# Kernel optimization log

Measured on AMD Instinct MI355X. Metric: run time of the kernel, lower is better.

The kernel has to match this reference:

```python
import jax, jax.numpy as jnp
import numpy as np

VOCAB = 1024
D = 1024  # predictor_dim
B = 32
U = 512
NULL_INDEX = 0


def setup_inputs() -> dict:
    key = jax.random.key(0)
    ks = jax.random.split(key, 9)
    s = 1.0 / np.sqrt(D)
    return {
        "y": jax.random.randint(ks[0], (B, U), 0, VOCAB, dtype=jnp.int32),
        "embed_table": jax.random.normal(ks[1], (VOCAB, D), jnp.float32) * s,
        "Wx": jax.random.normal(ks[2], (D, 3 * D), jnp.float32) * s,  # input kernel [z|r|h]
        "Wh": jax.random.normal(ks[3], (D, 3 * D), jnp.float32) * s,  # recurrent kernel [z|r|h]
        "bx": jnp.zeros((3 * D,), jnp.float32),  # input bias (reset_after=True)
        "bh": jnp.zeros((3 * D,), jnp.float32),  # recurrent bias (reset_after=True)
        "Wd": jax.random.normal(ks[4], (D, D), jnp.float32) * s,
        "bd": jnp.zeros((D,), jnp.float32),
        "h0": jax.random.normal(ks[5], (D,), jnp.float32),  # self.initial_state
    }


def _gru_scan(tokens, embed_table, Wx, Wh, bx, bh, h0_b):
    # tokens: [B, T] int; returns hidden states [B, T, D]
    x = embed_table[tokens]                       # [B, T, D]
    # Precompute all input projections outside the recurrence (one big GEMM)
    xp = jnp.einsum("btd,de->bte", x, Wx) + bx    # [B, T, 3D]
    xp = jnp.moveaxis(xp, 1, 0)                   # [T, B, 3D]

    def step(h, xp_t):
        hp = h @ Wh + bh                          # [B, 3D], reset_after=True
        xz, xr, xh = jnp.split(xp_t, 3, axis=-1)
        hz, hr, hh = jnp.split(hp, 3, axis=-1)
        z = jax.nn.sigmoid(xz + hz)
        r = jax.nn.sigmoid(xr + hr)
        hcand = jnp.tanh(xh + r * hh)
        h_new = z * h + (1.0 - z) * hcand
        return h_new, h_new

    _, hs = jax.lax.scan(step, h0_b, xp)          # hs: [T, B, D]
    return jnp.moveaxis(hs, 0, 1)                 # [B, T, D]


def reference(y, embed_table, Wx, Wh, bx, bh, Wd, bd, h0):
    Bn = y.shape[0]
    start = jnp.full((Bn, 1), NULL_INDEX, dtype=y.dtype)
    tokens = jnp.concatenate([start, y], axis=1)  # [B, U+1]
    h0_b = jnp.broadcast_to(h0, (Bn, D))
    hs = _gru_scan(tokens, embed_table, Wx, Wh, bx, bh, h0_b)  # [B, U+1, D]
    outs = jnp.einsum("btd,de->bte", hs, Wd) + bd
    return outs
```

## Files before the change

### kernel.cpp

```cpp
#include <hip/hip_runtime.h>
#include <hip/hip_bf16.h>
#include <cstdint>

typedef __bf16 bf16;
typedef __bf16 bf16x8 __attribute__((ext_vector_type(8)));
typedef float  f32x4  __attribute__((ext_vector_type(4)));
typedef uint32_t u32x4 __attribute__((ext_vector_type(4)));

#define D_DIM   1024
#define ND      3072
#define B_SZ    32
#define U_SZ    512
#define T_SZ    513
#define M_REAL  (B_SZ * T_SZ)
#define WXS_LD  1032
#define A_LD    1032
#define XP_LD   20

#define AGENT __HIP_MEMORY_SCOPE_AGENT

__device__ __forceinline__ f32x4 mfma16(bf16x8 a, bf16x8 b, f32x4 c) {
    return __builtin_amdgcn_mfma_f32_16x16x32_bf16(a, b, c, 0, 0, 0);
}

struct bfpair { bf16x8 hi, lo; };

__device__ __forceinline__ bfpair split8(const float* p) {
    f32x4 a = *(const f32x4*)p;
    f32x4 b = *(const f32x4*)(p + 4);
    bfpair r;
#pragma unroll
    for (int j = 0; j < 4; ++j) {
        r.hi[j] = (bf16)a[j];
        r.lo[j] = (bf16)(a[j] - (float)r.hi[j]);
        r.hi[4 + j] = (bf16)b[j];
        r.lo[4 + j] = (bf16)(b[j] - (float)r.hi[4 + j]);
    }
    return r;
}

__device__ __forceinline__ bf16x8 cvt8(const float* p) {
    f32x4 a = *(const f32x4*)p;
    f32x4 b = *(const f32x4*)(p + 4);
    bf16x8 r;
#pragma unroll
    for (int j = 0; j < 4; ++j) { r[j] = (bf16)a[j]; r[4 + j] = (bf16)b[j]; }
    return r;
}

__device__ __forceinline__ bfpair unpack8(const uint32_t* p) {
    u32x4 a = *(const u32x4*)p;
    u32x4 b = *(const u32x4*)(p + 4);
    union { uint32_t u[4]; bf16x8 v; } H, L;
    H.u[0] = __builtin_amdgcn_perm(a.y, a.x, 0x05040100u);
    H.u[1] = __builtin_amdgcn_perm(a.w, a.z, 0x05040100u);
    H.u[2] = __builtin_amdgcn_perm(b.y, b.x, 0x05040100u);
    H.u[3] = __builtin_amdgcn_perm(b.w, b.z, 0x05040100u);
    L.u[0] = __builtin_amdgcn_perm(a.y, a.x, 0x07060302u);
    L.u[1] = __builtin_amdgcn_perm(a.w, a.z, 0x07060302u);
    L.u[2] = __builtin_amdgcn_perm(b.y, b.x, 0x07060302u);
    L.u[3] = __builtin_amdgcn_perm(b.w, b.z, 0x07060302u);
    bfpair r; r.hi = H.v; r.lo = L.v;
    return r;
}

__global__ void transpose_split(const float* __restrict__ in,
                                bf16* __restrict__ out_hi, bf16* __restrict__ out_lo,
                                int R, int C) {
    __shared__ float tile[32][33];
    const int c0 = blockIdx.x * 32, r0 = blockIdx.y * 32;
    const int tx = threadIdx.x, ty = threadIdx.y;
    for (int i = 0; i < 32; i += 8)
        tile[ty + i][tx] = in[(size_t)(r0 + ty + i) * C + c0 + tx];
    __syncthreads();
    for (int i = 0; i < 32; i += 8) {
        const float v  = tile[tx][ty + i];
        const bf16  hi = (bf16)v;
        out_hi[(size_t)(c0 + ty + i) * R + r0 + tx] = hi;
        out_lo[(size_t)(c0 + ty + i) * R + r0 + tx] = (bf16)(v - (float)hi);
    }
}

__global__ __launch_bounds__(256, 1)
void gru_scan(const float* __restrict__ Wx,    const float* __restrict__ Wh,
              const float* __restrict__ bx,    const float* __restrict__ bh,
              const float* __restrict__ h0,    const float* __restrict__ embed,
              const int* __restrict__ y,       uint32_t* __restrict__ ghs,
              int* __restrict__ flags)
{
    __shared__ __align__(16) bf16 WxS[48 * WXS_LD];
    __shared__ __align__(16) float xpx[2][96 * XP_LD];
    __shared__ __align__(16) float bxs[3][16], bhs[3][16];

    const int tid  = threadIdx.x;
    const int wave = tid >> 6, lane = tid & 63;
    const int quad = lane >> 4, l15 = lane & 15;
    const int n0 = blockIdx.x * 16;
    int* slots = flags;

    for (int idx = tid; idx < 3 * 1024 * 16; idx += 256) {
        const int cl = idx & 15;
        const int k  = (idx >> 4) & 1023;
        const int g  = idx >> 14;
        WxS[(g * 16 + cl) * WXS_LD + k] = (bf16)Wx[(size_t)k * ND + g * D_DIM + n0 + cl];
    }
    if (tid < 48) {
        bxs[tid >> 4][tid & 15] = bx[(tid >> 4) * D_DIM + n0 + (tid & 15)];
        bhs[tid >> 4][tid & 15] = bh[(tid >> 4) * D_DIM + n0 + (tid & 15)];
    }

    bf16x8 bregZ[32], bregR[32], bregH[32];
    if (wave < 2) {
#pragma unroll
        for (int ks = 0; ks < 32; ++ks) {
            bf16x8 vz, vr, vh;
#pragma unroll
            for (int j = 0; j < 8; ++j) {
                const size_t krow = (size_t)(ks * 32 + quad * 8 + j) * ND + n0 + l15;
                vz[j] = (bf16)Wh[krow];
                vr[j] = (bf16)Wh[krow + D_DIM];
                vh[j] = (bf16)Wh[krow + 2 * D_DIM];
            }
            bregZ[ks] = vz; bregR[ks] = vr; bregH[ks] = vh;
        }
    }

    const int batch = (wave & 1) * 16 + l15;
    f32x4 holdv = *(const f32x4*)(h0 + n0 + quad * 4);
    unsigned long long junk = 0;

    __syncthreads();

    if (wave >= 2) {
        const float* xrow = embed + quad * 8;
        f32x4 ax0 = {}, ax1 = {}, ax2 = {};
#pragma unroll
        for (int ks = 0; ks < 32; ++ks) {
            bf16x8 xa = cvt8(xrow + ks * 32);
            bf16x8 w0 = *(const bf16x8*)(WxS + (l15)      * WXS_LD + ks * 32 + quad * 8);
            bf16x8 w1 = *(const bf16x8*)(WxS + (16 + l15) * WXS_LD + ks * 32 + quad * 8);
            bf16x8 w2 = *(const bf16x8*)(WxS + (32 + l15) * WXS_LD + ks * 32 + quad * 8);
            ax0 = mfma16(w0, xa, ax0);
            ax1 = mfma16(w1, xa, ax1);
            ax2 = mfma16(w2, xa, ax2);
        }
        *(f32x4*)(xpx[0] + (batch)      * XP_LD + quad * 4) = ax0;
        *(f32x4*)(xpx[0] + (32 + batch) * XP_LD + quad * 4) = ax1;
        *(f32x4*)(xpx[0] + (64 + batch) * XP_LD + quad * 4) = ax2;
    }
    __syncthreads();

    for (int t = 0; t < T_SZ; ++t) {
        if (wave < 2) {
            f32x4 azh = {}, azl = {}, arh = {}, arl = {}, ahh = {}, ahl = {};
            if (t == 0) {
                const float* hrow = h0 + quad * 8;
#pragma unroll
                for (int ks = 0; ks < 32; ++ks) {
                    bfpair h8 = split8(hrow + ks * 32);
                    azh = mfma16(bregZ[ks], h8.hi, azh);
                    azl = mfma16(bregZ[ks], h8.lo, azl);
                    arh = mfma16(bregR[ks], h8.hi, arh);
                    arl = mfma16(bregR[ks], h8.lo, arl);
                    ahh = mfma16(bregH[ks], h8.hi, ahh);
                    ahl = mfma16(bregH[ks], h8.lo, ahl);
                }
            } else {
                const uint32_t* hrow = ghs
                    + ((size_t)batch * T_SZ + (t - 1)) * D_DIM + quad * 8;
#pragma unroll
                for (int ks = 0; ks < 32; ++ks) {
                    bfpair h8 = unpack8(hrow + ks * 32);
                    azh = mfma16(bregZ[ks], h8.hi, azh);
                    azl = mfma16(bregZ[ks], h8.lo, azl);
                    arh = mfma16(bregR[ks], h8.hi, arh);
                    arl = mfma16(bregR[ks], h8.lo, arl);
                    ahh = mfma16(bregH[ks], h8.hi, ahh);
                    ahl = mfma16(bregH[ks], h8.lo, ahl);
                }
            }

            const int p = t & 1;
            const f32x4 xz = *(const f32x4*)(xpx[p] + (batch)      * XP_LD + quad * 4);
            const f32x4 xr = *(const f32x4*)(xpx[p] + (32 + batch) * XP_LD + quad * 4);
            const f32x4 xh = *(const f32x4*)(xpx[p] + (64 + batch) * XP_LD + quad * 4);
            const f32x4 bxz = *(const f32x4*)(&bxs[0][quad * 4]);
            const f32x4 bxr = *(const f32x4*)(&bxs[1][quad * 4]);
            const f32x4 bxh = *(const f32x4*)(&bxs[2][quad * 4]);
            const f32x4 bhz = *(const f32x4*)(&bhs[0][quad * 4]);
            const f32x4 bhr = *(const f32x4*)(&bhs[1][quad * 4]);
            const f32x4 bhh = *(const f32x4*)(&bhs[2][quad * 4]);
            uint32_t pk[4];
#pragma unroll
            for (int i = 0; i < 4; ++i) {
                const float hz  = azh[i] + azl[i] + bhz[i];
                const float hr  = arh[i] + arl[i] + bhr[i];
                const float hhv = ahh[i] + ahl[i] + bhh[i];
                const float z  = 1.f / (1.f + __expf(-(xz[i] + bxz[i] + hz)));
                const float r  = 1.f / (1.f + __expf(-(xr[i] + bxr[i] + hr)));
                const float pa = xh[i] + bxh[i] + r * hhv;
                const float hc = 1.f - 2.f / (__expf(2.f * pa) + 1.f);
                const float hn = z * holdv[i] + (1.f - z) * hc;
                holdv[i] = hn;
                const bf16 hi = (bf16)hn;
                const bf16 lo = (bf16)(hn - (float)hi);
                pk[i] = (uint32_t)__builtin_bit_cast(uint16_t, hi)
                      | ((uint32_t)__builtin_bit_cast(uint16_t, lo) << 16);
            }
            const unsigned long long e0 = (unsigned long long)pk[0]
                                        | ((unsigned long long)pk[1] << 32);
            const unsigned long long e1 = (unsigned long long)pk[2]
                                        | ((unsigned long long)pk[3] << 32);
            unsigned long long* dst = (unsigned long long*)
                (ghs + ((size_t)batch * T_SZ + t) * D_DIM + n0 + quad * 4);
            junk ^= __hip_atomic_exchange(dst,     e0, __ATOMIC_RELAXED, AGENT);
            junk ^= __hip_atomic_exchange(dst + 1, e1, __ATOMIC_RELAXED, AGENT);
        } else if (t < U_SZ) {
            const int tok = y[batch * U_SZ + t] & 1023;
            const float* xrow = embed + (size_t)tok * D_DIM + quad * 8;
            const int p = (t + 1) & 1;
            f32x4 ax0 = {}, ax1 = {}, ax2 = {};
#pragma unroll
            for (int ks = 0; ks < 32; ++ks) {
                bf16x8 xa = cvt8(xrow + ks * 32);
                bf16x8 w0 = *(const bf16x8*)(WxS + (l15)      * WXS_LD + ks * 32 + quad * 8);
                bf16x8 w1 = *(const bf16x8*)(WxS + (16 + l15) * WXS_LD + ks * 32 + quad * 8);
                bf16x8 w2 = *(const bf16x8*)(WxS + (32 + l15) * WXS_LD + ks * 32 + quad * 8);
                ax0 = mfma16(w0, xa, ax0);
                ax1 = mfma16(w1, xa, ax1);
                ax2 = mfma16(w2, xa, ax2);
            }
            *(f32x4*)(xpx[p] + (batch)      * XP_LD + quad * 4) = ax0;
            *(f32x4*)(xpx[p] + (32 + batch) * XP_LD + quad * 4) = ax1;
            *(f32x4*)(xpx[p] + (64 + batch) * XP_LD + quad * 4) = ax2;
        }

        __syncthreads();

        if (t + 1 < T_SZ) {
            const int tv = t + 1;
            if (tid == 0)
                __hip_atomic_store(slots + (blockIdx.x << 4), tv,
                                   __ATOMIC_RELAXED, AGENT);
            if (wave < 2) {
                int s;
                do {
                    s = __hip_atomic_load(slots + (lane << 4),
                                          __ATOMIC_RELAXED, AGENT);
                } while (__any(s < tv));
            }
        }
    }

    if (junk == 0xDEADBEEFDEADBEEFull) flags[1023] = 1;
}

__global__ __launch_bounds__(256, 1)
void gemm_rows_inplace(float* __restrict__ C,
                       const bf16* __restrict__ WdTh, const bf16* __restrict__ WdTl,
                       const float* __restrict__ bd)
{
    __shared__ __align__(16) bf16 Ah[32 * A_LD];
    __shared__ __align__(16) bf16 Al[32 * A_LD];
    const int tid  = threadIdx.x;
    const int wave = tid >> 6, lane = tid & 63;
    const int quad = lane >> 4, l15 = lane & 15;
    const size_t r0 = (size_t)blockIdx.x * 32;
    const uint32_t* Cw = (const uint32_t*)C;

    for (int idx = tid; idx < 32 * 128; idx += 256) {
        const int r = idx >> 7, ch = idx & 127;
        bfpair p = unpack8(Cw + (r0 + r) * D_DIM + ch * 8);
        *(bf16x8*)(Ah + r * A_LD + ch * 8) = p.hi;
        *(bf16x8*)(Al + r * A_LD + ch * 8) = p.lo;
    }
    __syncthreads();

    f32x4 acc[2][16] = {};
    const int nbase = wave * 256;
    for (int ks = 0; ks < 32; ++ks) {
        bf16x8 a0h = *(const bf16x8*)(Ah + (l15)      * A_LD + ks * 32 + quad * 8);
        bf16x8 a0l = *(const bf16x8*)(Al + (l15)      * A_LD + ks * 32 + quad * 8);
        bf16x8 a1h = *(const bf16x8*)(Ah + (16 + l15) * A_LD + ks * 32 + quad * 8);
        bf16x8 a1l = *(const bf16x8*)(Al + (16 + l15) * A_LD + ks * 32 + quad * 8);
#pragma unroll
        for (int nt = 0; nt < 16; ++nt) {
            const size_t boff = (size_t)(nbase + nt * 16 + l15) * D_DIM + ks * 32 + quad * 8;
            bf16x8 bhv = *(const bf16x8*)(WdTh + boff);
            bf16x8 blv = *(const bf16x8*)(WdTl + boff);
            acc[0][nt] = mfma16(a0h, bhv, acc[0][nt]);
            acc[0][nt] = mfma16(a0l, bhv, acc[0][nt]);
            acc[0][nt] = mfma16(a0h, blv, acc[0][nt]);
            acc[1][nt] = mfma16(a1h, bhv, acc[1][nt]);
            acc[1][nt] = mfma16(a1l, bhv, acc[1][nt]);
            acc[1][nt] = mfma16(a1h, blv, acc[1][nt]);
        }
    }

#pragma unroll
    for (int nt = 0; nt < 16; ++nt) {
        const int col = nbase + nt * 16 + l15;
        const float bvl = bd[col];
#pragma unroll
        for (int mt = 0; mt < 2; ++mt)
#pragma unroll
            for (int i = 0; i < 4; ++i)
                C[(r0 + mt * 16 + quad * 4 + i) * D_DIM + col] =
                    acc[mt][nt][i] + bvl;
    }
}

extern "C" void kernel_launch(void* const* d_in, const int* in_sizes, int n_in,
                              void* d_out, int out_size, void* d_ws, size_t ws_size,
                              hipStream_t stream) {
    (void)in_sizes; (void)n_in; (void)out_size; (void)ws_size;
    const int*   y     = (const int*)  d_in[0];
    const float* embed = (const float*)d_in[1];
    const float* Wx    = (const float*)d_in[2];
    const float* Wh    = (const float*)d_in[3];
    const float* bx    = (const float*)d_in[4];
    const float* bh    = (const float*)d_in[5];
    const float* Wd    = (const float*)d_in[6];
    const float* bd    = (const float*)d_in[7];
    const float* h0    = (const float*)d_in[8];
    float* out = (float*)d_out;

    bf16* WdTh = (bf16*)d_ws;
    bf16* WdTl = WdTh + (size_t)D_DIM * D_DIM;
    int* flags = (int*)((char*)d_ws + (size_t)D_DIM * D_DIM * 4);

    hipMemsetAsync(flags, 0, 8192, stream);

    transpose_split<<<dim3(D_DIM / 32, D_DIM / 32), dim3(32, 8), 0, stream>>>(
        Wd, WdTh, WdTl, D_DIM, D_DIM);

    gru_scan<<<64, 256, 0, stream>>>(Wx, Wh, bx, bh, h0, embed, y,
                                     (uint32_t*)out, flags);

    gemm_rows_inplace<<<M_REAL / 32, 256, 0, stream>>>(out, WdTh, WdTl, bd);
}
```

Baseline: 8.286 ms.

## Split recurrent K dimension across two waves per batch group with LDS reduction

```diff
diff --git a/kernel.cpp b/kernel.cpp
--- a/kernel.cpp
+++ b/kernel.cpp
@@ -81,7 +81,7 @@
     }
 }
 
-__global__ __launch_bounds__(256, 1)
+__global__ __launch_bounds__(384, 1)
 void gru_scan(const float* __restrict__ Wx,    const float* __restrict__ Wh,
               const float* __restrict__ bx,    const float* __restrict__ bh,
               const float* __restrict__ h0,    const float* __restrict__ embed,
@@ -90,6 +90,7 @@
 {
     __shared__ __align__(16) bf16 WxS[48 * WXS_LD];
     __shared__ __align__(16) float xpx[2][96 * XP_LD];
+    __shared__ __align__(16) float pP[2][3][16][20];
     __shared__ __align__(16) float bxs[3][16], bhs[3][16];
 
     const int tid  = threadIdx.x;
@@ -98,7 +99,7 @@
     const int n0 = blockIdx.x * 16;
     int* slots = flags;
 
-    for (int idx = tid; idx < 3 * 1024 * 16; idx += 256) {
+    for (int idx = tid; idx < 3 * 1024 * 16; idx += 384) {
         const int cl = idx & 15;
         const int k  = (idx >> 4) & 1023;
         const int g  = idx >> 14;
@@ -109,29 +110,33 @@
         bhs[tid >> 4][tid & 15] = bh[(tid >> 4) * D_DIM + n0 + (tid & 15)];
     }
 
-    bf16x8 bregZ[32], bregR[32], bregH[32];
-    if (wave < 2) {
-#pragma unroll
-        for (int ks = 0; ks < 32; ++ks) {
+    const int khalf = wave & 1;
+    const int grp   = (wave >> 1) & 1;
+    const int batch = (wave < 4) ? grp * 16 + l15 : (wave & 1) * 16 + l15;
+
+    bf16x8 bregZ[16], bregR[16], bregH[16];
+    if (wave < 4) {
+#pragma unroll
+        for (int kk = 0; kk < 16; ++kk) {
             bf16x8 vz, vr, vh;
 #pragma unroll
             for (int j = 0; j < 8; ++j) {
-                const size_t krow = (size_t)(ks * 32 + quad * 8 + j) * ND + n0 + l15;
+                const size_t krow =
+                    (size_t)(khalf * 512 + kk * 32 + quad * 8 + j) * ND + n0 + l15;
                 vz[j] = (bf16)Wh[krow];
                 vr[j] = (bf16)Wh[krow + D_DIM];
                 vh[j] = (bf16)Wh[krow + 2 * D_DIM];
             }
-            bregZ[ks] = vz; bregR[ks] = vr; bregH[ks] = vh;
-        }
-    }
-
-    const int batch = (wave & 1) * 16 + l15;
+            bregZ[kk] = vz; bregR[kk] = vr; bregH[kk] = vh;
+        }
+    }
+
     f32x4 holdv = *(const f32x4*)(h0 + n0 + quad * 4);
     unsigned long long junk = 0;
 
     __syncthreads();
 
-    if (wave >= 2) {
+    if (wave >= 4) {
         const float* xrow = embed + quad * 8;
         f32x4 ax0 = {}, ax1 = {}, ax2 = {};
 #pragma unroll
@@ -151,36 +156,69 @@
     __syncthreads();
 
     for (int t = 0; t < T_SZ; ++t) {
-        if (wave < 2) {
+        f32x4 sz = {}, sr = {}, sh = {};
+
+        if (wave < 4) {
             f32x4 azh = {}, azl = {}, arh = {}, arl = {}, ahh = {}, ahl = {};
             if (t == 0) {
-                const float* hrow = h0 + quad * 8;
-#pragma unroll
-                for (int ks = 0; ks < 32; ++ks) {
-                    bfpair h8 = split8(hrow + ks * 32);
-                    azh = mfma16(bregZ[ks], h8.hi, azh);
-                    azl = mfma16(bregZ[ks], h8.lo, azl);
-                    arh = mfma16(bregR[ks], h8.hi, arh);
-                    arl = mfma16(bregR[ks], h8.lo, arl);
-                    ahh = mfma16(bregH[ks], h8.hi, ahh);
-                    ahl = mfma16(bregH[ks], h8.lo, ahl);
+                const float* hrow = h0 + khalf * 512 + quad * 8;
+#pragma unroll
+                for (int kk = 0; kk < 16; ++kk) {
+                    bfpair h8 = split8(hrow + kk * 32);
+                    azh = mfma16(bregZ[kk], h8.hi, azh);
+                    azl = mfma16(bregZ[kk], h8.lo, azl);
+                    arh = mfma16(bregR[kk], h8.hi, arh);
+                    arl = mfma16(bregR[kk], h8.lo, arl);
+                    ahh = mfma16(bregH[kk], h8.hi, ahh);
+                    ahl = mfma16(bregH[kk], h8.lo, ahl);
                 }
             } else {
                 const uint32_t* hrow = ghs
-                    + ((size_t)batch * T_SZ + (t - 1)) * D_DIM + quad * 8;
-#pragma unroll
-                for (int ks = 0; ks < 32; ++ks) {
-                    bfpair h8 = unpack8(hrow + ks * 32);
-                    azh = mfma16(bregZ[ks], h8.hi, azh);
-                    azl = mfma16(bregZ[ks], h8.lo, azl);
-                    arh = mfma16(bregR[ks], h8.hi, arh);
-                    arl = mfma16(bregR[ks], h8.lo, arl);
-                    ahh = mfma16(bregH[ks], h8.hi, ahh);
-                    ahl = mfma16(bregH[ks], h8.lo, ahl);
+                    + ((size_t)batch * T_SZ + (t - 1)) * D_DIM + khalf * 512 + quad * 8;
+#pragma unroll
+                for (int kk = 0; kk < 16; ++kk) {
+                    bfpair h8 = unpack8(hrow + kk * 32);
+                    azh = mfma16(bregZ[kk], h8.hi, azh);
+                    azl = mfma16(bregZ[kk], h8.lo, azl);
+                    arh = mfma16(bregR[kk], h8.hi, arh);
+                    arl = mfma16(bregR[kk], h8.lo, arl);
+                    ahh = mfma16(bregH[kk], h8.hi, ahh);
+                    ahl = mfma16(bregH[kk], h8.lo, ahl);
                 }
             }
-
+            sz = azh + azl; sr = arh + arl; sh = ahh + ahl;
+            if (khalf) {
+                *(f32x4*)&pP[grp][0][l15][quad * 4] = sz;
+                *(f32x4*)&pP[grp][1][l15][quad * 4] = sr;
+                *(f32x4*)&pP[grp][2][l15][quad * 4] = sh;
+            }
+        } else if (t < U_SZ) {
+            const int tok = y[batch * U_SZ + t] & 1023;
+            const float* xrow = embed + (size_t)tok * D_DIM + quad * 8;
+            const int p = (t + 1) & 1;
+            f32x4 ax0 = {}, ax1 = {}, ax2 = {};
+#pragma unroll
+            for (int ks = 0; ks < 32; ++ks) {
+                bf16x8 xa = cvt8(xrow + ks * 32);
+                bf16x8 w0 = *(const bf16x8*)(WxS + (l15)      * WXS_LD + ks * 32 + quad * 8);
+                bf16x8 w1 = *(const bf16x8*)(WxS + (16 + l15) * WXS_LD + ks * 32 + quad * 8);
+                bf16x8 w2 = *(const bf16x8*)(WxS + (32 + l15) * WXS_LD + ks * 32 + quad * 8);
+                ax0 = mfma16(w0, xa, ax0);
+                ax1 = mfma16(w1, xa, ax1);
+                ax2 = mfma16(w2, xa, ax2);
+            }
+            *(f32x4*)(xpx[p] + (batch)      * XP_LD + quad * 4) = ax0;
+            *(f32x4*)(xpx[p] + (32 + batch) * XP_LD + quad * 4) = ax1;
+            *(f32x4*)(xpx[p] + (64 + batch) * XP_LD + quad * 4) = ax2;
+        }
+
+        __syncthreads();
+
+        if (wave < 4 && khalf == 0) {
             const int p = t & 1;
+            const f32x4 qz = *(const f32x4*)&pP[grp][0][l15][quad * 4];
+            const f32x4 qr = *(const f32x4*)&pP[grp][1][l15][quad * 4];
+            const f32x4 qh = *(const f32x4*)&pP[grp][2][l15][quad * 4];
             const f32x4 xz = *(const f32x4*)(xpx[p] + (batch)      * XP_LD + quad * 4);
             const f32x4 xr = *(const f32x4*)(xpx[p] + (32 + batch) * XP_LD + quad * 4);
             const f32x4 xh = *(const f32x4*)(xpx[p] + (64 + batch) * XP_LD + quad * 4);
@@ -193,9 +231,9 @@
             uint32_t pk[4];
 #pragma unroll
             for (int i = 0; i < 4; ++i) {
-                const float hz  = azh[i] + azl[i] + bhz[i];
-                const float hr  = arh[i] + arl[i] + bhr[i];
-                const float hhv = ahh[i] + ahl[i] + bhh[i];
+                const float hz  = sz[i] + qz[i] + bhz[i];
+                const float hr  = sr[i] + qr[i] + bhr[i];
+                const float hhv = sh[i] + qh[i] + bhh[i];
                 const float z  = 1.f / (1.f + __expf(-(xz[i] + bxz[i] + hz)));
                 const float r  = 1.f / (1.f + __expf(-(xr[i] + bxr[i] + hr)));
                 const float pa = xh[i] + bxh[i] + r * hhv;
@@ -215,24 +253,6 @@
                 (ghs + ((size_t)batch * T_SZ + t) * D_DIM + n0 + quad * 4);
             junk ^= __hip_atomic_exchange(dst,     e0, __ATOMIC_RELAXED, AGENT);
             junk ^= __hip_atomic_exchange(dst + 1, e1, __ATOMIC_RELAXED, AGENT);
-        } else if (t < U_SZ) {
-            const int tok = y[batch * U_SZ + t] & 1023;
-            const float* xrow = embed + (size_t)tok * D_DIM + quad * 8;
-            const int p = (t + 1) & 1;
-            f32x4 ax0 = {}, ax1 = {}, ax2 = {};
-#pragma unroll
-            for (int ks = 0; ks < 32; ++ks) {
-                bf16x8 xa = cvt8(xrow + ks * 32);
-                bf16x8 w0 = *(const bf16x8*)(WxS + (l15)      * WXS_LD + ks * 32 + quad * 8);
-                bf16x8 w1 = *(const bf16x8*)(WxS + (16 + l15) * WXS_LD + ks * 32 + quad * 8);
-                bf16x8 w2 = *(const bf16x8*)(WxS + (32 + l15) * WXS_LD + ks * 32 + quad * 8);
-                ax0 = mfma16(w0, xa, ax0);
-                ax1 = mfma16(w1, xa, ax1);
-                ax2 = mfma16(w2, xa, ax2);
-            }
-            *(f32x4*)(xpx[p] + (batch)      * XP_LD + quad * 4) = ax0;
-            *(f32x4*)(xpx[p] + (32 + batch) * XP_LD + quad * 4) = ax1;
-            *(f32x4*)(xpx[p] + (64 + batch) * XP_LD + quad * 4) = ax2;
         }
 
         __syncthreads();
@@ -242,7 +262,7 @@
             if (tid == 0)
                 __hip_atomic_store(slots + (blockIdx.x << 4), tv,
                                    __ATOMIC_RELAXED, AGENT);
-            if (wave < 2) {
+            if (wave < 4) {
                 int s;
                 do {
                     s = __hip_atomic_load(slots + (lane << 4),
@@ -334,7 +354,7 @@
     transpose_split<<<dim3(D_DIM / 32, D_DIM / 32), dim3(32, 8), 0, stream>>>(
         Wd, WdTh, WdTl, D_DIM, D_DIM);
 
-    gru_scan<<<64, 256, 0, stream>>>(Wx, Wh, bx, bh, h0, embed, y,
+    gru_scan<<<64, 384, 0, stream>>>(Wx, Wh, bx, bh, h0, embed, y,
                                      (uint32_t*)out, flags);
 
     gemm_rows_inplace<<<M_REAL / 32, 256, 0, stream>>>(out, WdTh, WdTl, bd);
```

After: 8.530 ms. 3.0% more time.
